# Kernel tuning notes

Hardware: AMD Instinct MI355X
Metric: run time of the kernel (lower is better)

The kernel has to match this reference:

```python
import jax, jax.numpy as jnp
import numpy as np

B, L, D, H = 4, 2048, 1024, 16
HD = D // H
EPS = 1e-5


def _layernorm(x, g, b):
    mu = jnp.mean(x, axis=-1, keepdims=True)
    var = jnp.mean(jnp.square(x - mu), axis=-1, keepdims=True)
    return (x - mu) * jax.lax.rsqrt(var + EPS) * g + b


def _rotate_half(x):
    x1, x2 = jnp.split(x, 2, axis=-1)
    return jnp.concatenate([-x2, x1], axis=-1)


def setup_inputs() -> dict:
    key = jax.random.key(0)
    ks = jax.random.split(key, 12)
    s = 0.02
    return {
        "x": jax.random.normal(ks[0], (B, L, D), jnp.float32),
        "pos_cos": jax.random.uniform(ks[1], (B, L, D), jnp.float32),
        "pos_sin": jax.random.uniform(ks[2], (B, L, D), jnp.float32),
        "attn_mask": jnp.zeros((B, L), jnp.float32),
        "Wq": jax.random.normal(ks[3], (D, D), jnp.float32) * s,
        "Wk": jax.random.normal(ks[4], (D, D), jnp.float32) * s,
        "Wv": jax.random.normal(ks[5], (D, D), jnp.float32) * s,
        "Wo": jax.random.normal(ks[6], (D, D), jnp.float32) * s,
        "W1": jax.random.normal(ks[7], (D, 2 * D), jnp.float32) * s,
        "W2": jax.random.normal(ks[8], (D, D), jnp.float32) * s,
        "g1": jnp.ones((D,), jnp.float32),
        "b1": jnp.zeros((D,), jnp.float32),
        "g2": jnp.ones((D,), jnp.float32),
        "b2": jnp.zeros((D,), jnp.float32),
    }


def reference(x, pos_cos, pos_sin, attn_mask, Wq, Wk, Wv, Wo, W1, W2, g1, b1, g2, b2):
    # --- attention sublayer (pre-LN) ---
    residual = x
    xn = _layernorm(x, g1, b1)
    split_heads = lambda t: t.reshape(B, L, H, HD).transpose(0, 2, 1, 3)  # [B,H,L,hd]
    q = split_heads(xn @ Wq)
    k = split_heads(xn @ Wk)
    v = split_heads(xn @ Wv)
    cos = split_heads(pos_cos)
    sin = split_heads(pos_sin)
    q = q * cos + _rotate_half(q) * sin
    k = k * cos + _rotate_half(k) * sin
    scores = jnp.einsum('bhqd,bhkd->bhqk', q, k) / np.float32(np.sqrt(HD))
    scores = scores + attn_mask[:, None, None, :]  # additive mask over keys
    probs = jax.nn.softmax(scores, axis=-1)
    ctx = jnp.einsum('bhqk,bhkd->bhqd', probs, v)
    ctx = ctx.transpose(0, 2, 1, 3).reshape(B, L, D)
    x = residual + ctx @ Wo
    # --- SwiGLU FFN sublayer (pre-LN) ---
    residual = x
    xn = _layernorm(x, g2, b2)
    h = xn @ W1
    x1, x2 = h[..., :D], h[..., D:]
    ffn = (jax.nn.silu(x1) * x2) @ W2
    return residual + ffn
```

## Files before the change

### kernel.cpp

```cpp
#include <hip/hip_runtime.h>
#include <hip/hip_bf16.h>

typedef unsigned short ushort_t;
typedef short short8 __attribute__((ext_vector_type(8)));
typedef unsigned short u16x4 __attribute__((ext_vector_type(4)));
typedef float f32x4 __attribute__((ext_vector_type(4)));
typedef int int2v __attribute__((ext_vector_type(2)));
typedef int int4v __attribute__((ext_vector_type(4)));

#define MFMA_BF16 __builtin_amdgcn_mfma_f32_16x16x32_bf16

#define GLDS16(g, l) __builtin_amdgcn_global_load_lds( \
    (__attribute__((address_space(1))) void*)(g), \
    (__attribute__((address_space(3))) void*)(l), 16, 0, 0)

__device__ __forceinline__ unsigned short f2bf(float f) {
  union { float f; unsigned u; } v; v.f = f;
  unsigned r = v.u + 0x7FFFu + ((v.u >> 16) & 1u);
  return (unsigned short)(r >> 16);
}
__device__ __forceinline__ float bf2f(unsigned short h) {
  union { unsigned u; float f; } v; v.u = ((unsigned)h) << 16;
  return v.f;
}
__device__ __forceinline__ unsigned pack_bf2(float a, float b) {
  __hip_bfloat162 t = __float22bfloat162_rn(float2{a, b});
  union { __hip_bfloat162 h; unsigned u; } v; v.h = t;
  return v.u;
}
__device__ __forceinline__ float exp2_raw(float x) {
  float r;
  asm volatile("v_exp_f32 %0, %1" : "=v"(r) : "v"(x));
  return r;
}

#define BB 4
#define LL 2048
#define DD 1024
#define HH 16
#define HD 64
#define NROW (BB * LL)
#define LOG2E 1.4426950408889634f

template <int PERM>
__global__ __launch_bounds__(256) void wconv(const float* __restrict__ W,
                                             ushort_t* __restrict__ WT,
                                             int R, int C) {
  __shared__ float tile[32][33];
  const int ct = blockIdx.x * 32, rt = blockIdx.y * 32;
  const int tx = threadIdx.x & 31, ty = threadIdx.x >> 5;
#pragma unroll
  for (int j = 0; j < 4; ++j)
    tile[ty + j * 8][tx] = W[(size_t)(rt + ty + j * 8) * C + ct + tx];
  __syncthreads();
  int orow0 = ct;
  if (PERM)
    orow0 = (ct < 1024) ? ((ct >> 5) * 64) : ((((ct - 1024) >> 5) * 64) + 32);
#pragma unroll
  for (int j = 0; j < 4; ++j)
    WT[(size_t)(orow0 + ty + j * 8) * R + rt + tx] = f2bf(tile[tx][ty + j * 8]);
}

template <int BIN>
__global__ __launch_bounds__(256) void ln_kernel(const void* __restrict__ xin,
                                                 const float* __restrict__ g,
                                                 const float* __restrict__ bt,
                                                 ushort_t* __restrict__ out) {
  const int row = blockIdx.x, t = threadIdx.x;
  f32x4 v;
  if (BIN) {
    const u16x4 hv =
        *(const u16x4*)((const ushort_t*)xin + (size_t)row * DD + t * 4);
    v[0] = bf2f(hv[0]); v[1] = bf2f(hv[1]);
    v[2] = bf2f(hv[2]); v[3] = bf2f(hv[3]);
  } else {
    v = *(const f32x4*)((const float*)xin + (size_t)row * DD + t * 4);
  }
  float s = v[0] + v[1] + v[2] + v[3];
  float sq = v[0] * v[0] + v[1] * v[1] + v[2] * v[2] + v[3] * v[3];
#pragma unroll
  for (int off = 1; off < 64; off <<= 1) {
    s += __shfl_xor(s, off);
    sq += __shfl_xor(sq, off);
  }
  __shared__ float aw[4], aq[4];
  if ((t & 63) == 0) { aw[t >> 6] = s; aq[t >> 6] = sq; }
  __syncthreads();
  s = aw[0] + aw[1] + aw[2] + aw[3];
  sq = aq[0] + aq[1] + aq[2] + aq[3];
  const float mu = s * (1.f / DD);
  const float var = sq * (1.f / DD) - mu * mu;
  const float rs = rsqrtf(var + 1e-5f);
  u16x4 o;
#pragma unroll
  for (int j = 0; j < 4; ++j) {
    const int c = t * 4 + j;
    o[j] = f2bf((v[j] - mu) * rs * g[c] + bt[c]);
  }
  *(u16x4*)(out + (size_t)row * DD + t * 4) = o;
}

template <int EPI>
__global__ __launch_bounds__(256) void gemm_bt(const ushort_t* __restrict__ A,
                                               const ushort_t* __restrict__ BT,
                                               ushort_t* __restrict__ Cb,
                                               float* __restrict__ Cf,
                                               const float* __restrict__ residf,
                                               const ushort_t* __restrict__ residb,
                                               int M, int N, int K) {
  __shared__ ushort_t As[128 * 32];
  __shared__ ushort_t Bs[128 * 32];
  const int tid = threadIdx.x;
  const int lane = tid & 63;
  const int w = tid >> 6;
  const int wr = w >> 1, wc = w & 1;
  const int nwg = gridDim.x * gridDim.y;
  const int orig = blockIdx.y * gridDim.x + blockIdx.x;
  const int wg = (orig & 7) * (nwg >> 3) + (orig >> 3);
  const int bm = (wg / gridDim.x) * 128, bn = (wg % gridDim.x) * 128;
  const int lrow = lane >> 2;
  const int lcol = (lane & 3) * 8;
  const int fr = lane & 15;
  const int fo = (lane >> 4) * 8;
  f32x4 acc[4][4];
#pragma unroll
  for (int m = 0; m < 4; ++m)
#pragma unroll
    for (int n = 0; n < 4; ++n) acc[m][n] = (f32x4){0.f, 0.f, 0.f, 0.f};

  const int nk = K >> 5;
  for (int kt = 0; kt < nk; ++kt) {
    __syncthreads();
#pragma unroll
    for (int c = 0; c < 2; ++c) {
      const int seg = c * 4 + w;
      const int row = seg * 16 + lrow;
      GLDS16(A + (size_t)(bm + row) * K + kt * 32 + lcol, &As[seg * 512]);
      GLDS16(BT + (size_t)(bn + row) * K + kt * 32 + lcol, &Bs[seg * 512]);
    }
    asm volatile("s_waitcnt vmcnt(0)" ::: "memory");
    __syncthreads();
    short8 af[4], bf_[4];
#pragma unroll
    for (int m = 0; m < 4; ++m)
      af[m] = *(const short8*)&As[(wr * 64 + m * 16 + fr) * 32 + fo];
#pragma unroll
    for (int n = 0; n < 4; ++n)
      bf_[n] = *(const short8*)&Bs[(wc * 64 + n * 16 + fr) * 32 + fo];
#pragma unroll
    for (int m = 0; m < 4; ++m)
#pragma unroll
      for (int n = 0; n < 4; ++n)
        acc[m][n] = MFMA_BF16(af[m], bf_[n], acc[m][n], 0, 0, 0);
  }
  const int r0 = (lane >> 4) * 4;
#pragma unroll
  for (int m = 0; m < 4; ++m)
#pragma unroll
    for (int n = 0; n < 4; ++n)
#pragma unroll
      for (int r = 0; r < 4; ++r) {
        const int gr = bm + wr * 64 + m * 16 + r0 + r;
        const int gc = bn + wc * 64 + n * 16 + fr;
        const size_t o = (size_t)gr * N + gc;
        if (EPI == 1) Cb[o] = f2bf(residf[o] + acc[m][n][r]);
        else          Cf[o] = bf2f(residb[o]) + acc[m][n][r];
      }
}

template <int EPI>
__global__ __launch_bounds__(256) void gemm_f(
    const ushort_t* __restrict__ A, const ushort_t* __restrict__ BT,
    const float* __restrict__ pcos, const float* __restrict__ psin,
    ushort_t* __restrict__ qh, ushort_t* __restrict__ kh,
    ushort_t* __restrict__ vt, ushort_t* __restrict__ gact,
    int M, int N, int K) {
  __shared__ ushort_t As[128 * 32];
  __shared__ ushort_t Bs[128 * 32];
  const int tid = threadIdx.x;
  const int lane = tid & 63;
  const int w = tid >> 6;
  const int wr = w >> 1, wc = w & 1;
  const int nwg = gridDim.x * gridDim.y;
  const int orig = blockIdx.y * gridDim.x + blockIdx.x;
  const int wg = (orig & 7) * (nwg >> 3) + (orig >> 3);
  const int bm = (wg / gridDim.x) * 128, bn = (wg % gridDim.x) * 128;
  const int lrow = lane >> 2;
  const int lcol = (lane & 3) * 8;
  const int fr = lane & 15;
  const int hi = lane >> 4;
  const int fo = hi * 8;
  f32x4 acc[4][4];
#pragma unroll
  for (int m = 0; m < 4; ++m)
#pragma unroll
    for (int n = 0; n < 4; ++n) acc[m][n] = (f32x4){0.f, 0.f, 0.f, 0.f};

  const int nk = K >> 5;
  for (int kt = 0; kt < nk; ++kt) {
    __syncthreads();
#pragma unroll
    for (int c = 0; c < 2; ++c) {
      const int seg = c * 4 + w;
      const int row = seg * 16 + lrow;
      GLDS16(A + (size_t)(bm + row) * K + kt * 32 + lcol, &As[seg * 512]);
      GLDS16(BT + (size_t)(bn + row) * K + kt * 32 + lcol, &Bs[seg * 512]);
    }
    asm volatile("s_waitcnt vmcnt(0)" ::: "memory");
    __syncthreads();
    short8 af[4], bf_[4];
#pragma unroll
    for (int m = 0; m < 4; ++m)
      af[m] = *(const short8*)&As[(wr * 64 + m * 16 + fr) * 32 + fo];
#pragma unroll
    for (int n = 0; n < 4; ++n)
      bf_[n] = *(const short8*)&Bs[(wc * 64 + n * 16 + fr) * 32 + fo];
#pragma unroll
    for (int m = 0; m < 4; ++m)
#pragma unroll
      for (int n = 0; n < 4; ++n)
        acc[m][n] = MFMA_BF16(af[m], bf_[n], acc[m][n], 0, 0, 0);
  }

  if (EPI == 1) {
    const int gcol = bn + wc * 64;
    const int region = gcol >> 10;
    const int h = (gcol & 1023) >> 6;
    const int b = bm >> 11;
    if (region < 2) {
      const float qs = (region == 0) ? 0.125f : 1.0f;
      ushort_t* dstbuf = (region == 0) ? qh : kh;
      const int dbase = h * 64;
#pragma unroll
      for (int m = 0; m < 4; ++m) {
        const int gr0 = bm + wr * 64 + m * 16 + hi * 4;
#pragma unroll
        for (int r = 0; r < 4; ++r) {
          const int gr = gr0 + r;
          const int l = gr & 2047;
          const float* pcr = pcos + (size_t)gr * DD + dbase;
          const float* psr = psin + (size_t)gr * DD + dbase;
          ushort_t* dst = dstbuf + ((size_t)(b * HH + h) * LL + l) * HD;
#pragma unroll
          for (int n = 0; n < 2; ++n) {
            const int dlo = n * 16 + fr;
            const float xlo = acc[m][n][r], xhi = acc[m][n + 2][r];
            dst[dlo] = f2bf((xlo * pcr[dlo] - xhi * psr[dlo]) * qs);
            dst[dlo + 32] = f2bf((xhi * pcr[dlo + 32] + xlo * psr[dlo + 32]) * qs);
          }
        }
      }
    } else {
      const size_t bhv = (size_t)(b * HH + h);
      const int l0 = (bm & 2047) + wr * 64;
      const int lt = l0 >> 6;
#pragma unroll
      for (int m = 0; m < 4; ++m) {
        const int slotb = 32 * (m >> 1) + 8 * hi + 4 * (m & 1);
#pragma unroll
        for (int n = 0; n < 4; ++n) {
          const int hd = n * 16 + fr;
          u16x4 wv;
          wv[0] = f2bf(acc[m][n][0]);
          wv[1] = f2bf(acc[m][n][1]);
          wv[2] = f2bf(acc[m][n][2]);
          wv[3] = f2bf(acc[m][n][3]);
          *(u16x4*)(vt + (bhv * HD + hd) * LL + lt * 64 + slotb) = wv;
        }
      }
    }
  } else {
    const int jbase = ((bn + wc * 64) >> 6) * 32;
#pragma unroll
    for (int m = 0; m < 4; ++m) {
      const int gr0 = bm + wr * 64 + m * 16 + hi * 4;
#pragma unroll
      for (int r = 0; r < 4; ++r) {
        ushort_t* dst = gact + (size_t)(gr0 + r) * DD + jbase;
#pragma unroll
        for (int n = 0; n < 2; ++n) {
          const float x1 = acc[m][n][r];
          const float x2 = acc[m][n + 2][r];
          dst[n * 16 + fr] = f2bf(x1 / (1.f + __expf(-x1)) * x2);
        }
      }
    }
  }
}

__global__ __launch_bounds__(512) void attn_kernel(
    const ushort_t* __restrict__ qh, const ushort_t* __restrict__ kh,
    const ushort_t* __restrict__ vt, const float* __restrict__ mask,
    ushort_t* __restrict__ ctx) {
  const int tid = threadIdx.x, lane = tid & 63, w = tid >> 6;
  const int bh = blockIdx.y, b = bh >> 4, h = bh & 15;
  const int q0 = blockIdx.x * 256;
  __shared__ ushort_t Ks[2][64 * 64];
  __shared__ ushort_t Vs[2][64 * 64];
  const int fr = lane & 15;
  const int hi = lane >> 4;
  const int fo = hi * 8;
  short8 qf[2][2];
#pragma unroll
  for (int st = 0; st < 2; ++st) {
    const int qrow = q0 + w * 32 + st * 16 + fr;
    const size_t qoff = ((size_t)bh * LL + qrow) * HD + fo;
    qf[st][0] = *(const short8*)(qh + qoff);
    qf[st][1] = *(const short8*)(qh + qoff + 32);
  }
  short8 ones;
#pragma unroll
  for (int i = 0; i < 8; ++i) ones[i] = (short)0x3F80;

  f32x4 oacc[2][4];
  f32x4 lacc[2];
#pragma unroll
  for (int st = 0; st < 2; ++st) {
    lacc[st] = (f32x4){0.f, 0.f, 0.f, 0.f};
#pragma unroll
    for (int m = 0; m < 4; ++m) oacc[st][m] = (f32x4){0.f, 0.f, 0.f, 0.f};
  }

  const int lrow = lane >> 3;
  const int lcs = ((lane & 7) ^ lrow) * 8;

#define STAGE_KV(kt, bb)                                                      \
  {                                                                           \
    const int rr = w * 8 + lrow;                                              \
    GLDS16(kh + ((size_t)bh * LL + (kt) * 64 + rr) * HD + lcs,                \
           &Ks[bb][w * 512]);                                                 \
    GLDS16(vt + ((size_t)bh * HD + rr) * LL + (kt) * 64 + lcs,                \
           &Vs[bb][w * 512]);                                                 \
  }

  const float* mrow = mask + (size_t)b * LL;
  f32x4 mkc[4];
#pragma unroll
  for (int n = 0; n < 4; ++n)
    mkc[n] = *(const f32x4*)(mrow + n * 16 + hi * 4);

  STAGE_KV(0, 0);
  asm volatile("s_waitcnt vmcnt(0)" ::: "memory");
  __syncthreads();
  int cur = 0;
  const int NT = LL / 64;
  for (int kt = 0; kt < NT; ++kt) {
    f32x4 mkn[4];
    if (kt + 1 < NT) {
      STAGE_KV(kt + 1, cur ^ 1);
#pragma unroll
      for (int n = 0; n < 4; ++n)
        mkn[n] = *(const f32x4*)(mrow + (kt + 1) * 64 + n * 16 + hi * 4);
    } else {
#pragma unroll
      for (int n = 0; n < 4; ++n) mkn[n] = mkc[n];
    }

#pragma unroll
    for (int st = 0; st < 2; ++st) {
      f32x4 s[4];
#pragma unroll
      for (int n = 0; n < 4; ++n) s[n] = mkc[n];
      __builtin_amdgcn_s_setprio(1);
#pragma unroll
      for (int n = 0; n < 4; ++n) {
        const int krow = n * 16 + fr;
#pragma unroll
        for (int c = 0; c < 2; ++c) {
          const int col = (c * 32 + fo) ^ ((fr & 7) * 8);
          const short8 kf = *(const short8*)&Ks[cur][krow * 64 + col];
          s[n] = MFMA_BF16(kf, qf[st][c], s[n], 0, 0, 0);
        }
      }
      __builtin_amdgcn_s_setprio(0);
      unsigned pk[4][2];
#pragma unroll
      for (int n = 0; n < 4; ++n) {
        const float p0 = exp2_raw(s[n][0] * LOG2E);
        const float p1 = exp2_raw(s[n][1] * LOG2E);
        const float p2 = exp2_raw(s[n][2] * LOG2E);
        const float p3 = exp2_raw(s[n][3] * LOG2E);
        pk[n][0] = pack_bf2(p0, p1);
        pk[n][1] = pack_bf2(p2, p3);
      }
      __builtin_amdgcn_s_setprio(1);
#pragma unroll
      for (int c = 0; c < 2; ++c) {
        int4v pw = {(int)pk[2 * c][0], (int)pk[2 * c][1],
                    (int)pk[2 * c + 1][0], (int)pk[2 * c + 1][1]};
        union { int4v i; short8 s; } pf; pf.i = pw;
#pragma unroll
        for (int m = 0; m < 4; ++m) {
          const int row = m * 16 + fr;
          const int col = (c * 32 + fo) ^ ((fr & 7) * 8);
          const short8 vf = *(const short8*)&Vs[cur][row * 64 + col];
          oacc[st][m] = MFMA_BF16(vf, pf.s, oacc[st][m], 0, 0, 0);
        }
        lacc[st] = MFMA_BF16(ones, pf.s, lacc[st], 0, 0, 0);
      }
      __builtin_amdgcn_s_setprio(0);
    }
#pragma unroll
    for (int n = 0; n < 4; ++n) mkc[n] = mkn[n];
    asm volatile("s_waitcnt vmcnt(0)" ::: "memory");
    __syncthreads();
    cur ^= 1;
  }
#pragma unroll
  for (int st = 0; st < 2; ++st) {
    const float inv = 1.f / lacc[st][0];
    const int q = q0 + w * 32 + st * 16 + fr;
    ushort_t* dst = ctx + ((size_t)b * LL + q) * DD + h * 64 + hi * 4;
#pragma unroll
    for (int m = 0; m < 4; ++m) {
      int2v val;
      val[0] = (int)pack_bf2(oacc[st][m][0] * inv, oacc[st][m][1] * inv);
      val[1] = (int)pack_bf2(oacc[st][m][2] * inv, oacc[st][m][3] * inv);
      *(int2v*)(dst + m * 16) = val;
    }
  }
#undef STAGE_KV
}

extern "C" void kernel_launch(void* const* d_in, const int* in_sizes, int n_in,
                              void* d_out, int out_size, void* d_ws,
                              size_t ws_size, hipStream_t stream) {
  const float* x = (const float*)d_in[0];
  const float* pcos = (const float*)d_in[1];
  const float* psin = (const float*)d_in[2];
  const float* mask = (const float*)d_in[3];
  const float* Wq = (const float*)d_in[4];
  const float* Wk = (const float*)d_in[5];
  const float* Wv = (const float*)d_in[6];
  const float* Wo = (const float*)d_in[7];
  const float* W1 = (const float*)d_in[8];
  const float* W2 = (const float*)d_in[9];
  const float* g1 = (const float*)d_in[10];
  const float* b1 = (const float*)d_in[11];
  const float* g2 = (const float*)d_in[12];
  const float* b2 = (const float*)d_in[13];
  float* out = (float*)d_out;
  char* ws = (char*)d_ws;

  ushort_t* WQKVT = (ushort_t*)(ws);
  ushort_t* WOT = (ushort_t*)(ws + 6291456);
  ushort_t* W1T = (ushort_t*)(ws + 8388608);
  ushort_t* W2T = (ushort_t*)(ws + 12582912);
  ushort_t* XN = (ushort_t*)(ws + 14680064);
  ushort_t* GACT = (ushort_t*)(ws + 31457280 + 33554432);
  ushort_t* QH = (ushort_t*)(ws + 81788928);
  ushort_t* KH = (ushort_t*)(ws + 98566144);
  ushort_t* VT = (ushort_t*)(ws + 115343360);
  ushort_t* CTX = (ushort_t*)(ws + 132120576);
  ushort_t* XMIDB = (ushort_t*)(ws + 148897792);

  wconv<0><<<dim3(32, 32), 256, 0, stream>>>(Wq, WQKVT, 1024, 1024);
  wconv<0><<<dim3(32, 32), 256, 0, stream>>>(Wk, WQKVT + 1024 * 1024, 1024, 1024);
  wconv<0><<<dim3(32, 32), 256, 0, stream>>>(Wv, WQKVT + 2 * 1024 * 1024, 1024, 1024);
  wconv<0><<<dim3(32, 32), 256, 0, stream>>>(Wo, WOT, 1024, 1024);
  wconv<1><<<dim3(64, 32), 256, 0, stream>>>(W1, W1T, 1024, 2048);
  wconv<0><<<dim3(32, 32), 256, 0, stream>>>(W2, W2T, 1024, 1024);

  ln_kernel<0><<<NROW, 256, 0, stream>>>(x, g1, b1, XN);
  gemm_f<1><<<dim3(24, 64), 256, 0, stream>>>(XN, WQKVT, pcos, psin, QH, KH,
                                              VT, nullptr, NROW, 3072, 1024);
  attn_kernel<<<dim3(8, 64), 512, 0, stream>>>(QH, KH, VT, mask, CTX);
  gemm_bt<1><<<dim3(8, 64), 256, 0, stream>>>(CTX, WOT, XMIDB, nullptr, x,
                                              nullptr, NROW, 1024, 1024);
  ln_kernel<1><<<NROW, 256, 0, stream>>>(XMIDB, g2, b2, XN);
  gemm_f<2><<<dim3(16, 64), 256, 0, stream>>>(XN, W1T, nullptr, nullptr,
                                              nullptr, nullptr, nullptr, GACT,
                                              NROW, 2048, 1024);
  gemm_bt<2><<<dim3(8, 64), 256, 0, stream>>>(GACT, W2T, nullptr, out, nullptr,
                                              XMIDB, NROW, 1024, 1024);
}
```

Baseline: 377.4 us.

## Halve attention query tile per block and load 128-key tiles without prefetch

The attention kernel now gives each wave 16 query rows instead of 32, so twice as many blocks are launched (16x64 grid), which raises parallelism and cuts register pressure. The double-buffered prefetch pipeline is replaced by a synchronous scheme. Each iteration loads a 128-key tile into both LDS buffers, waits for it, then computes. This drops the overlap of global loads with compute, and each K/V tile is reloaded by twice as many blocks, doubling K/V traffic per query.

```diff
diff --git a/kernel.cpp b/kernel.cpp
--- a/kernel.cpp
+++ b/kernel.cpp
@@ -294,73 +294,52 @@
     ushort_t* __restrict__ ctx) {
   const int tid = threadIdx.x, lane = tid & 63, w = tid >> 6;
   const int bh = blockIdx.y, b = bh >> 4, h = bh & 15;
-  const int q0 = blockIdx.x * 256;
+  const int q0 = blockIdx.x * 128;
   __shared__ ushort_t Ks[2][64 * 64];
   __shared__ ushort_t Vs[2][64 * 64];
   const int fr = lane & 15;
   const int hi = lane >> 4;
   const int fo = hi * 8;
-  short8 qf[2][2];
-#pragma unroll
-  for (int st = 0; st < 2; ++st) {
-    const int qrow = q0 + w * 32 + st * 16 + fr;
-    const size_t qoff = ((size_t)bh * LL + qrow) * HD + fo;
-    qf[st][0] = *(const short8*)(qh + qoff);
-    qf[st][1] = *(const short8*)(qh + qoff + 32);
-  }
+  const int qrow = q0 + w * 16 + fr;
+  const size_t qoff = ((size_t)bh * LL + qrow) * HD + fo;
+  const short8 qf0 = *(const short8*)(qh + qoff);
+  const short8 qf1 = *(const short8*)(qh + qoff + 32);
   short8 ones;
 #pragma unroll
   for (int i = 0; i < 8; ++i) ones[i] = (short)0x3F80;
 
-  f32x4 oacc[2][4];
-  f32x4 lacc[2];
-#pragma unroll
-  for (int st = 0; st < 2; ++st) {
-    lacc[st] = (f32x4){0.f, 0.f, 0.f, 0.f};
-#pragma unroll
-    for (int m = 0; m < 4; ++m) oacc[st][m] = (f32x4){0.f, 0.f, 0.f, 0.f};
-  }
+  f32x4 oacc[4];
+  f32x4 lacc = (f32x4){0.f, 0.f, 0.f, 0.f};
+#pragma unroll
+  for (int m = 0; m < 4; ++m) oacc[m] = (f32x4){0.f, 0.f, 0.f, 0.f};
 
   const int lrow = lane >> 3;
   const int lcs = ((lane & 7) ^ lrow) * 8;
-
-#define STAGE_KV(kt, bb)                                                      \
-  {                                                                           \
-    const int rr = w * 8 + lrow;                                              \
-    GLDS16(kh + ((size_t)bh * LL + (kt) * 64 + rr) * HD + lcs,                \
-           &Ks[bb][w * 512]);                                                 \
-    GLDS16(vt + ((size_t)bh * HD + rr) * LL + (kt) * 64 + lcs,                \
-           &Vs[bb][w * 512]);                                                 \
-  }
+  const int rr = w * 8 + lrow;
 
   const float* mrow = mask + (size_t)b * LL;
-  f32x4 mkc[4];
-#pragma unroll
-  for (int n = 0; n < 4; ++n)
-    mkc[n] = *(const f32x4*)(mrow + n * 16 + hi * 4);
-
-  STAGE_KV(0, 0);
-  asm volatile("s_waitcnt vmcnt(0)" ::: "memory");
-  __syncthreads();
-  int cur = 0;
-  const int NT = LL / 64;
+
+  const int NT = LL / 128;
   for (int kt = 0; kt < NT; ++kt) {
-    f32x4 mkn[4];
-    if (kt + 1 < NT) {
-      STAGE_KV(kt + 1, cur ^ 1);
-#pragma unroll
-      for (int n = 0; n < 4; ++n)
-        mkn[n] = *(const f32x4*)(mrow + (kt + 1) * 64 + n * 16 + hi * 4);
-    } else {
-#pragma unroll
-      for (int n = 0; n < 4; ++n) mkn[n] = mkc[n];
-    }
-
-#pragma unroll
-    for (int st = 0; st < 2; ++st) {
+    __syncthreads();
+    GLDS16(kh + ((size_t)bh * LL + kt * 128 + rr) * HD + lcs, &Ks[0][w * 512]);
+    GLDS16(kh + ((size_t)bh * LL + kt * 128 + 64 + rr) * HD + lcs,
+           &Ks[1][w * 512]);
+    GLDS16(vt + ((size_t)bh * HD + rr) * LL + kt * 128 + lcs, &Vs[0][w * 512]);
+    GLDS16(vt + ((size_t)bh * HD + rr) * LL + kt * 128 + 64 + lcs,
+           &Vs[1][w * 512]);
+    f32x4 mk[8];
+#pragma unroll
+    for (int n = 0; n < 8; ++n)
+      mk[n] = *(const f32x4*)(mrow + kt * 128 + n * 16 + hi * 4);
+    asm volatile("s_waitcnt vmcnt(0)" ::: "memory");
+    __syncthreads();
+
+#pragma unroll
+    for (int sub = 0; sub < 2; ++sub) {
       f32x4 s[4];
 #pragma unroll
-      for (int n = 0; n < 4; ++n) s[n] = mkc[n];
+      for (int n = 0; n < 4; ++n) s[n] = mk[sub * 4 + n];
       __builtin_amdgcn_s_setprio(1);
 #pragma unroll
       for (int n = 0; n < 4; ++n) {
@@ -368,8 +347,8 @@
 #pragma unroll
         for (int c = 0; c < 2; ++c) {
           const int col = (c * 32 + fo) ^ ((fr & 7) * 8);
-          const short8 kf = *(const short8*)&Ks[cur][krow * 64 + col];
-          s[n] = MFMA_BF16(kf, qf[st][c], s[n], 0, 0, 0);
+          const short8 kf = *(const short8*)&Ks[sub][krow * 64 + col];
+          s[n] = MFMA_BF16(kf, c ? qf1 : qf0, s[n], 0, 0, 0);
         }
       }
       __builtin_amdgcn_s_setprio(0);
@@ -393,33 +372,24 @@
         for (int m = 0; m < 4; ++m) {
           const int row = m * 16 + fr;
           const int col = (c * 32 + fo) ^ ((fr & 7) * 8);
-          const short8 vf = *(const short8*)&Vs[cur][row * 64 + col];
-          oacc[st][m] = MFMA_BF16(vf, pf.s, oacc[st][m], 0, 0, 0);
+          const short8 vf = *(const short8*)&Vs[sub][row * 64 + col];
+          oacc[m] = MFMA_BF16(vf, pf.s, oacc[m], 0, 0, 0);
         }
-        lacc[st] = MFMA_BF16(ones, pf.s, lacc[st], 0, 0, 0);
+        lacc = MFMA_BF16(ones, pf.s, lacc, 0, 0, 0);
       }
       __builtin_amdgcn_s_setprio(0);
     }
-#pragma unroll
-    for (int n = 0; n < 4; ++n) mkc[n] = mkn[n];
-    asm volatile("s_waitcnt vmcnt(0)" ::: "memory");
-    __syncthreads();
-    cur ^= 1;
-  }
-#pragma unroll
-  for (int st = 0; st < 2; ++st) {
-    const float inv = 1.f / lacc[st][0];
-    const int q = q0 + w * 32 + st * 16 + fr;
-    ushort_t* dst = ctx + ((size_t)b * LL + q) * DD + h * 64 + hi * 4;
-#pragma unroll
-    for (int m = 0; m < 4; ++m) {
-      int2v val;
-      val[0] = (int)pack_bf2(oacc[st][m][0] * inv, oacc[st][m][1] * inv);
-      val[1] = (int)pack_bf2(oacc[st][m][2] * inv, oacc[st][m][3] * inv);
-      *(int2v*)(dst + m * 16) = val;
-    }
-  }
-#undef STAGE_KV
+  }
+  const float inv = 1.f / lacc[0];
+  const int q = q0 + w * 16 + fr;
+  ushort_t* dst = ctx + ((size_t)b * LL + q) * DD + h * 64 + hi * 4;
+#pragma unroll
+  for (int m = 0; m < 4; ++m) {
+    int2v val;
+    val[0] = (int)pack_bf2(oacc[m][0] * inv, oacc[m][1] * inv);
+    val[1] = (int)pack_bf2(oacc[m][2] * inv, oacc[m][3] * inv);
+    *(int2v*)(dst + m * 16) = val;
+  }
 }
 
 extern "C" void kernel_launch(void* const* d_in, const int* in_sizes, int n_in,
@@ -464,7 +434,7 @@
   ln_kernel<0><<<NROW, 256, 0, stream>>>(x, g1, b1, XN);
   gemm_f<1><<<dim3(24, 64), 256, 0, stream>>>(XN, WQKVT, pcos, psin, QH, KH,
                                               VT, nullptr, NROW, 3072, 1024);
-  attn_kernel<<<dim3(8, 64), 512, 0, stream>>>(QH, KH, VT, mask, CTX);
+  attn_kernel<<<dim3(16, 64), 512, 0, stream>>>(QH, KH, VT, mask, CTX);
   gemm_bt<1><<<dim3(8, 64), 256, 0, stream>>>(CTX, WOT, XMIDB, nullptr, x,
                                               nullptr, NROW, 1024, 1024);
   ln_kernel<1><<<NROW, 256, 0, stream>>>(XMIDB, g2, b2, XN);
```

New measurement: 372.6 us. No clear change (-1.3%).
